# Performance work log

Measured on AMD Instinct MI355X. Metric: run time of the kernel, lower is better.

The kernel has to match this reference:

```python
import jax, jax.numpy as jnp
import numpy as np

B, N, F, H = 2, 2048, 1024, 16
HD = F // H
SQRT_D = float(np.sqrt(F))  # note: module scales by sqrt(in_c), not sqrt(head_dim)


def setup_inputs() -> dict:
    key = jax.random.key(0)
    ks = jax.random.split(key, 9)
    s = 1.0 / np.sqrt(F)
    mk = lambda k: jax.random.uniform(k, (F, F), jnp.float32, -s, s)
    mb = lambda k: jax.random.uniform(k, (F,), jnp.float32, -s, s)
    return {
        "x": jax.random.normal(ks[0], (B, N, F), jnp.float32),
        "Wq": mk(ks[1]), "bq": mb(ks[2]),
        "Wk": mk(ks[3]), "bk": mb(ks[4]),
        "Wv": mk(ks[5]), "bv": mb(ks[6]),
        "Wo": mk(ks[7]), "bo": mb(ks[8]),
    }


def reference(x, Wq, bq, Wk, bk, Wv, bv, Wo, bo):
    b, n, f = x.shape
    # projections (torch Linear: x @ W.T + b); view to (b, n, h, hd)
    q = (x @ Wq.T + bq).reshape(b, n, H, HD)
    k = (x @ Wk.T + bk).reshape(b, n, H, HD)
    v = (x @ Wv.T + bv).reshape(b, n, H, HD)
    score = jnp.einsum('bihd,bjhd->bhij', q, k)
    attn = jax.nn.softmax(score / SQRT_D, axis=-1)
    o = jnp.einsum('bhij,bjhd->bihd', attn, v).reshape(b, n, f)
    return o @ Wo.T + bo
```

## Files before the change

### kernel.cpp

```cpp
#include <hip/hip_runtime.h>
#include <hip/hip_bf16.h>
#include <stdint.h>
#include <stddef.h>

typedef __bf16 bf16;
typedef __attribute__((ext_vector_type(8))) __bf16 bf16x8;
typedef __attribute__((ext_vector_type(4))) __bf16 bf16x4;
typedef __attribute__((ext_vector_type(2))) __bf16 bf16x2;
typedef __attribute__((ext_vector_type(4))) float f32x4;

#define MFMA16(a, b, c) __builtin_amdgcn_mfma_f32_16x16x32_bf16(a, b, c, 0, 0, 0)

#define BB 2
#define SEQ 2048
#define FDIM 1024
#define NH 16
#define HD 64
#define M_TOK 4096
#define N_QKV 3072

#define CSC 0.04508422f

__device__ __forceinline__ void gll16(const bf16* g, bf16* l) {
    __builtin_amdgcn_global_load_lds(
        (const __attribute__((address_space(1))) void*)g,
        (__attribute__((address_space(3))) void*)l, 16, 0, 0);
}

__device__ __forceinline__ bf16 pack_bf16(float f) {
    uint32_t u = __builtin_bit_cast(uint32_t, f);
    uint16_t h = (uint16_t)((u + 0x8000u) >> 16);
    return __builtin_bit_cast(bf16, h);
}

__device__ __forceinline__ uint32_t pk2(float a, float b) {
#if __has_builtin(__builtin_amdgcn_cvt_pk_bf16_f32)
    bf16x2 t = __builtin_amdgcn_cvt_pk_bf16_f32(a, b);
    return __builtin_bit_cast(uint32_t, t);
#else
    uint32_t ua = __builtin_bit_cast(uint32_t, a) + 0x8000u;
    uint32_t ub = __builtin_bit_cast(uint32_t, b) + 0x8000u;
    return __builtin_amdgcn_perm(ub, ua, 0x07060302);
#endif
}

__global__ __launch_bounds__(256) void convert_k(
    const float* __restrict__ x,
    const float* __restrict__ Wq, const float* __restrict__ bq,
    const float* __restrict__ Wk, const float* __restrict__ bk,
    const float* __restrict__ Wv, const float* __restrict__ bv,
    const float* __restrict__ Wo,
    bf16* __restrict__ xb, bf16* __restrict__ Wcat, bf16* __restrict__ Wob,
    float* __restrict__ bcat)
{
    const int tid = blockIdx.x * blockDim.x + threadIdx.x;
    const int nt = gridDim.x * blockDim.x;
    const int NX4 = M_TOK * FDIM / 4;
    const int NW4 = FDIM * FDIM / 4;

    for (int i = tid; i < NX4; i += nt) {
        float4 v = ((const float4*)x)[i];
        bf16x4 o; o[0] = (bf16)v.x; o[1] = (bf16)v.y; o[2] = (bf16)v.z; o[3] = (bf16)v.w;
        ((bf16x4*)xb)[i] = o;
    }
    for (int i = tid; i < NW4; i += nt) {
        float4 v = ((const float4*)Wq)[i];
        bf16x4 o;
        o[0] = (bf16)(v.x * CSC); o[1] = (bf16)(v.y * CSC);
        o[2] = (bf16)(v.z * CSC); o[3] = (bf16)(v.w * CSC);
        ((bf16x4*)Wcat)[i] = o;
        v = ((const float4*)Wk)[i];
        o[0] = (bf16)v.x; o[1] = (bf16)v.y; o[2] = (bf16)v.z; o[3] = (bf16)v.w;
        ((bf16x4*)Wcat)[NW4 + i] = o;
        v = ((const float4*)Wv)[i];
        o[0] = (bf16)v.x; o[1] = (bf16)v.y; o[2] = (bf16)v.z; o[3] = (bf16)v.w;
        ((bf16x4*)Wcat)[2 * NW4 + i] = o;
        v = ((const float4*)Wo)[i];
        o[0] = (bf16)v.x; o[1] = (bf16)v.y; o[2] = (bf16)v.z; o[3] = (bf16)v.w;
        ((bf16x4*)Wob)[i] = o;
    }
    for (int i = tid; i < FDIM; i += nt) {
        bcat[i] = bq[i] * CSC;
        bcat[FDIM + i] = bk[i];
        bcat[2 * FDIM + i] = bv[i];
    }
}

template<int MT>
__global__ __launch_bounds__(256) void gemm_bt(
    const bf16* __restrict__ A,
    const bf16* __restrict__ Bw,
    const float* __restrict__ bias,
    bf16* __restrict__ Cb,
    float* __restrict__ Cf,
    bf16* __restrict__ VtOut,
    int M, int N, int K)
{
    constexpr int RI = MT / 32;
    __shared__ __align__(16) bf16 As[2][MT * 32];
    __shared__ __align__(16) bf16 Bs[2][128 * 32];

    const int tid = threadIdx.x;
    const int lane = tid & 63;
    const int wave = tid >> 6;
    const int m0 = blockIdx.y * MT;
    const int n0 = blockIdx.x * 128;
    const int wm = (wave >> 1) * (MT / 2);
    const int wn = (wave & 1) * 64;
    const int lrow = lane & 15;
    const int lk8 = (lane >> 4) * 8;

    f32x4 acc[RI][4] = {};

    const int srow = wave * 16 + (lane >> 2);
    const int scol = (lane & 3) * 8;
    const bf16* Ag = A + (size_t)(m0 + srow) * K + scol;
    const bf16* Bg = Bw + (size_t)(n0 + srow) * K + scol;
    const int wo = (wave * 16) * 32;

    gll16(Ag, &As[0][wo]);
    if (MT == 128) gll16(Ag + (size_t)64 * K, &As[0][wo + 2048]);
    gll16(Bg, &Bs[0][wo]);
    gll16(Bg + (size_t)64 * K, &Bs[0][wo + 2048]);

    for (int k0 = 0, it = 0; k0 < K; k0 += 32, ++it) {
        const int cur = it & 1;
        __syncthreads();

        if (k0 + 32 < K) {
            const int nxt = cur ^ 1;
            gll16(Ag + k0 + 32, &As[nxt][wo]);
            if (MT == 128) gll16(Ag + (size_t)64 * K + k0 + 32, &As[nxt][wo + 2048]);
            gll16(Bg + k0 + 32, &Bs[nxt][wo]);
            gll16(Bg + (size_t)64 * K + k0 + 32, &Bs[nxt][wo + 2048]);
        }

        bf16x8 af[RI], bfr[4];
#pragma unroll
        for (int s = 0; s < RI; ++s)
            af[s] = *(const bf16x8*)&As[cur][(wm + s * 16 + lrow) * 32 + lk8];
#pragma unroll
        for (int s = 0; s < 4; ++s)
            bfr[s] = *(const bf16x8*)&Bs[cur][(wn + s * 16 + lrow) * 32 + lk8];
#pragma unroll
        for (int i = 0; i < RI; ++i)
#pragma unroll
            for (int j = 0; j < 4; ++j)
                acc[i][j] = MFMA16(af[i], bfr[j], acc[i][j]);
    }

    const int r0 = (lane >> 4) * 4;
    if (MT == 128 && VtOut && n0 >= 2048) {
        const int bql = (m0 >> 11);
#pragma unroll
        for (int i = 0; i < RI; ++i) {
#pragma unroll
            for (int j = 0; j < 4; ++j) {
                const int col = n0 + wn + j * 16 + lrow;
                const float bsv = bias[col];
                const int vh = col - 2048;
                const int row = m0 + wm + i * 16 + r0;
                const int jj = row & (SEQ - 1);
                const int g = jj & 63;
                const int jj2 = (jj & ~63) | ((g >> 5) << 5)
                              | (((g >> 2) & 3) << 3) | (((g >> 4) & 1) << 2);
                bf16x4 vv;
#pragma unroll
                for (int r = 0; r < 4; ++r)
                    vv[r] = pack_bf16(acc[i][j][r] + bsv);
                *(bf16x4*)&VtOut[((size_t)bql * 16 * 64 + vh) * SEQ + jj2] = vv;
            }
        }
        return;
    }
#pragma unroll
    for (int i = 0; i < RI; ++i) {
#pragma unroll
        for (int j = 0; j < 4; ++j) {
            const int col = n0 + wn + j * 16 + lrow;
            const float bsv = bias[col];
#pragma unroll
            for (int r = 0; r < 4; ++r) {
                const int row = m0 + wm + i * 16 + r0 + r;
                const float v = acc[i][j][r] + bsv;
                if (Cb) Cb[(size_t)row * N + col] = pack_bf16(v);
                else    Cf[(size_t)row * N + col] = v;
            }
        }
    }
}

__global__ __launch_bounds__(256) void attn_k(
    const bf16* __restrict__ QKV,
    const bf16* __restrict__ Vt,
    bf16* __restrict__ O)
{
    const int bx = blockIdx.x;
    const int bh = (bx & 7) + 8 * ((bx >> 3) & 3);
    const int qblk = bx >> 5;
    const int b = bh >> 4;
    const int h = bh & 15;
    const int lane = threadIdx.x & 63;
    const int wave = threadIdx.x >> 6;
    const int lrow = lane & 15;
    const int quad = lane >> 4;
    const int lk8 = quad * 8;

    __shared__ __align__(16) bf16 Ks[2][2][128 * 32];
    __shared__ __align__(16) bf16 Vs[2][4][64 * 32];

    const size_t base = (size_t)b * SEQ * N_QKV;
    const bf16* Qp = QKV + base + h * HD;
    const bf16* Kp = QKV + base + FDIM + h * HD;
    const bf16* Vtp = Vt + (size_t)bh * HD * SEQ;

    const int qr0 = qblk * 128 + wave * 32;

    bf16x8 qf[2][2];
#pragma unroll
    for (int qt = 0; qt < 2; ++qt)
#pragma unroll
        for (int ks = 0; ks < 2; ++ks)
            qf[qt][ks] = *(const bf16x8*)(Qp + (size_t)(qr0 + qt * 16 + lrow) * N_QKV
                                          + ks * 32 + lk8);

    bf16x8 ones8;
#pragma unroll
    for (int e = 0; e < 8; ++e) ones8[e] = (bf16)1.0f;

    const f32x4 zf = {0.f, 0.f, 0.f, 0.f};

    f32x4 o[2][4] = {};
    f32x4 o4[2] = {};

    const int srow = wave * 16 + (lane >> 2);
    const int scol = (lane & 3) * 8;
    const bf16* kg = Kp + (size_t)srow * N_QKV + scol;
    const bf16* vg = Vtp + (size_t)srow * SEQ + scol;
    const int wo = (wave * 16) * 32;

    gll16(kg, &Ks[0][0][wo]);
    gll16(kg + 32, &Ks[0][1][wo]);
    gll16(kg + (size_t)64 * N_QKV, &Ks[0][0][wo + 2048]);
    gll16(kg + (size_t)64 * N_QKV + 32, &Ks[0][1][wo + 2048]);
    gll16(vg, &Vs[0][0][wo]);
    gll16(vg + 32, &Vs[0][1][wo]);
    gll16(vg + 64, &Vs[0][2][wo]);
    gll16(vg + 96, &Vs[0][3][wo]);
    kg += (size_t)128 * N_QKV;
    vg += 128;

    for (int jt = 0; jt < SEQ / 128; ++jt) {
        const int cur = jt & 1;
        __syncthreads();

        if (jt + 1 < SEQ / 128) {
            const int nxt = cur ^ 1;
            gll16(kg, &Ks[nxt][0][wo]);
            gll16(kg + 32, &Ks[nxt][1][wo]);
            gll16(kg + (size_t)64 * N_QKV, &Ks[nxt][0][wo + 2048]);
            gll16(kg + (size_t)64 * N_QKV + 32, &Ks[nxt][1][wo + 2048]);
            gll16(vg, &Vs[nxt][0][wo]);
            gll16(vg + 32, &Vs[nxt][1][wo]);
            gll16(vg + 64, &Vs[nxt][2][wo]);
            gll16(vg + 96, &Vs[nxt][3][wo]);
            kg += (size_t)128 * N_QKV;
            vg += 128;
        }

#pragma unroll
        for (int p = 0; p < 4; ++p) {
            f32x4 Sp[2][2];
            __builtin_amdgcn_s_setprio(1);
#pragma unroll
            for (int m = 0; m < 2; ++m) {
                const int jn = 2 * p + m;
                bf16x8 kb0 = *(const bf16x8*)&Ks[cur][0][(jn * 16 + lrow) * 32 + lk8];
                bf16x8 kb1 = *(const bf16x8*)&Ks[cur][1][(jn * 16 + lrow) * 32 + lk8];
                Sp[m][0] = MFMA16(kb0, qf[0][0], zf);
                Sp[m][0] = MFMA16(kb1, qf[0][1], Sp[m][0]);
                Sp[m][1] = MFMA16(kb0, qf[1][0], zf);
                Sp[m][1] = MFMA16(kb1, qf[1][1], Sp[m][1]);
            }
            __builtin_amdgcn_s_setprio(0);

            union { bf16x8 v; uint32_t d[4]; } pb[2];
#pragma unroll
            for (int qt = 0; qt < 2; ++qt) {
                const f32x4 s0 = Sp[0][qt];
                const f32x4 s1 = Sp[1][qt];
                pb[qt].d[0] = pk2(__builtin_amdgcn_exp2f(s0[0]),
                                  __builtin_amdgcn_exp2f(s0[1]));
                pb[qt].d[1] = pk2(__builtin_amdgcn_exp2f(s0[2]),
                                  __builtin_amdgcn_exp2f(s0[3]));
                pb[qt].d[2] = pk2(__builtin_amdgcn_exp2f(s1[0]),
                                  __builtin_amdgcn_exp2f(s1[1]));
                pb[qt].d[3] = pk2(__builtin_amdgcn_exp2f(s1[2]),
                                  __builtin_amdgcn_exp2f(s1[3]));
            }

            __builtin_amdgcn_s_setprio(1);
            o4[0] = MFMA16(ones8, pb[0].v, o4[0]);
            o4[1] = MFMA16(ones8, pb[1].v, o4[1]);
#pragma unroll
            for (int df = 0; df < 4; ++df) {
                bf16x8 vA = *(const bf16x8*)&Vs[cur][p][(df * 16 + lrow) * 32 + lk8];
                o[0][df] = MFMA16(vA, pb[0].v, o[0][df]);
                o[1][df] = MFMA16(vA, pb[1].v, o[1][df]);
            }
            __builtin_amdgcn_s_setprio(0);
        }
    }

#pragma unroll
    for (int qt = 0; qt < 2; ++qt) {
        const float inv = 1.0f / o4[qt][0];
        const int q = qr0 + qt * 16 + lrow;
#pragma unroll
        for (int df = 0; df < 4; ++df) {
            bf16x4 vv;
#pragma unroll
            for (int r = 0; r < 4; ++r)
                vv[r] = pack_bf16(o[qt][df][r] * inv);
            *(bf16x4*)&O[(size_t)(b * SEQ + q) * FDIM + h * HD + df * 16 + quad * 4] = vv;
        }
    }
}

extern "C" void kernel_launch(void* const* d_in, const int* in_sizes, int n_in,
                              void* d_out, int out_size, void* d_ws, size_t ws_size,
                              hipStream_t stream) {
    (void)in_sizes; (void)n_in; (void)out_size; (void)ws_size;
    const float* x  = (const float*)d_in[0];
    const float* Wq = (const float*)d_in[1];
    const float* bq = (const float*)d_in[2];
    const float* Wk = (const float*)d_in[3];
    const float* bk = (const float*)d_in[4];
    const float* Wv = (const float*)d_in[5];
    const float* bv = (const float*)d_in[6];
    const float* Wo = (const float*)d_in[7];
    const float* bo = (const float*)d_in[8];
    float* out = (float*)d_out;

    char* ws = (char*)d_ws;
    bf16* xb    = (bf16*)(ws);
    bf16* Wcat  = (bf16*)(ws + 8388608);
    bf16* Wob   = (bf16*)(ws + 14680064);
    float* bcat = (float*)(ws + 16777216);
    bf16* QKV   = (bf16*)(ws + 16789504);
    bf16* Vt    = (bf16*)(ws + 41955328);
    bf16* Ob    = xb;

    convert_k<<<dim3(1024), dim3(256), 0, stream>>>(x, Wq, bq, Wk, bk, Wv, bv, Wo,
                                                    xb, Wcat, Wob, bcat);
    gemm_bt<128><<<dim3(N_QKV / 128, M_TOK / 128), dim3(256), 0, stream>>>(
        xb, Wcat, bcat, QKV, nullptr, Vt, M_TOK, N_QKV, FDIM);
    attn_k<<<dim3((SEQ / 128) * BB * NH), dim3(256), 0, stream>>>(QKV, Vt, Ob);
    gemm_bt<64><<<dim3(FDIM / 128, M_TOK / 64), dim3(256), 0, stream>>>(
        Ob, Wob, bo, nullptr, out, nullptr, M_TOK, FDIM, FDIM);
}
```

Before: 190.5 us.

## Split attention key range across two wave groups with LDS reduction

The attention block grows from 4 to 8 waves. Each query group of 32 rows is now handled by two waves that each process half of the 32-key sub-tiles in every 128-key tile. The partial outputs and denominators are then combined through shared memory at the end. Cooperative K/V loads are redistributed so each wave issues half as many global-to-LDS loads. The goal is more waves per CU for latency hiding, at the cost of a final LDS reduction and synchronisation, plus register pressure from the launch bounds.

```diff
diff --git a/kernel.cpp b/kernel.cpp
--- a/kernel.cpp
+++ b/kernel.cpp
@@ -190,7 +190,7 @@
     }
 }
 
-__global__ __launch_bounds__(256) void attn_k(
+__global__ __launch_bounds__(512, 4) void attn_k(
     const bf16* __restrict__ QKV,
     const bf16* __restrict__ Vt,
     bf16* __restrict__ O)
@@ -202,6 +202,8 @@
     const int h = bh & 15;
     const int lane = threadIdx.x & 63;
     const int wave = threadIdx.x >> 6;
+    const int qg = wave & 3;
+    const int jp = wave >> 2;
     const int lrow = lane & 15;
     const int quad = lane >> 4;
     const int lk8 = quad * 8;
@@ -214,7 +216,7 @@
     const bf16* Kp = QKV + base + FDIM + h * HD;
     const bf16* Vtp = Vt + (size_t)bh * HD * SEQ;
 
-    const int qr0 = qblk * 128 + wave * 32;
+    const int qr0 = qblk * 128 + qg * 32;
 
     bf16x8 qf[2][2];
 #pragma unroll
@@ -236,17 +238,14 @@
     const int srow = wave * 16 + (lane >> 2);
     const int scol = (lane & 3) * 8;
     const bf16* kg = Kp + (size_t)srow * N_QKV + scol;
-    const bf16* vg = Vtp + (size_t)srow * SEQ + scol;
-    const int wo = (wave * 16) * 32;
-
-    gll16(kg, &Ks[0][0][wo]);
-    gll16(kg + 32, &Ks[0][1][wo]);
-    gll16(kg + (size_t)64 * N_QKV, &Ks[0][0][wo + 2048]);
-    gll16(kg + (size_t)64 * N_QKV + 32, &Ks[0][1][wo + 2048]);
-    gll16(vg, &Vs[0][0][wo]);
-    gll16(vg + 32, &Vs[0][1][wo]);
-    gll16(vg + 64, &Vs[0][2][wo]);
-    gll16(vg + 96, &Vs[0][3][wo]);
+    const int vsrow = qg * 16 + (lane >> 2);
+    const bf16* vg = Vtp + (size_t)vsrow * SEQ + jp * 32 + scol;
+    const int kwo = wave * 512;
+
+    gll16(kg,      &Ks[0][0][0] + kwo);
+    gll16(kg + 32, &Ks[0][1][0] + kwo);
+    gll16(vg,      &Vs[0][0][0] + kwo);
+    gll16(vg + 64, &Vs[0][2][0] + kwo);
     kg += (size_t)128 * N_QKV;
     vg += 128;
 
@@ -256,20 +255,17 @@
 
         if (jt + 1 < SEQ / 128) {
             const int nxt = cur ^ 1;
-            gll16(kg, &Ks[nxt][0][wo]);
-            gll16(kg + 32, &Ks[nxt][1][wo]);
-            gll16(kg + (size_t)64 * N_QKV, &Ks[nxt][0][wo + 2048]);
-            gll16(kg + (size_t)64 * N_QKV + 32, &Ks[nxt][1][wo + 2048]);
-            gll16(vg, &Vs[nxt][0][wo]);
-            gll16(vg + 32, &Vs[nxt][1][wo]);
-            gll16(vg + 64, &Vs[nxt][2][wo]);
-            gll16(vg + 96, &Vs[nxt][3][wo]);
+            gll16(kg,      &Ks[nxt][0][0] + kwo);
+            gll16(kg + 32, &Ks[nxt][1][0] + kwo);
+            gll16(vg,      &Vs[nxt][0][0] + kwo);
+            gll16(vg + 64, &Vs[nxt][2][0] + kwo);
             kg += (size_t)128 * N_QKV;
             vg += 128;
         }
 
 #pragma unroll
-        for (int p = 0; p < 4; ++p) {
+        for (int pp = 0; pp < 2; ++pp) {
+            const int p = (pp << 1) | jp;
             f32x4 Sp[2][2];
             __builtin_amdgcn_s_setprio(1);
 #pragma unroll
@@ -312,9 +308,35 @@
         }
     }
 
+    __syncthreads();
+    float* shO = (float*)Ks;
+    float* shS = (float*)Vs;
+    if (jp == 1) {
+#pragma unroll
+        for (int qt = 0; qt < 2; ++qt)
+#pragma unroll
+            for (int df = 0; df < 4; ++df)
+                *(f32x4*)&shO[((((qt * 4 + df) * 4) + qg) * 64 + lane) * 4] = o[qt][df];
+        shS[(qg * 64 + lane) * 2 + 0] = o4[0][0];
+        shS[(qg * 64 + lane) * 2 + 1] = o4[1][0];
+    }
+    __syncthreads();
+    if (jp == 1) return;
+
+#pragma unroll
+    for (int qt = 0; qt < 2; ++qt)
+#pragma unroll
+        for (int df = 0; df < 4; ++df) {
+            f32x4 t = *(const f32x4*)&shO[((((qt * 4 + df) * 4) + qg) * 64 + lane) * 4];
+            o[qt][df][0] += t[0]; o[qt][df][1] += t[1];
+            o[qt][df][2] += t[2]; o[qt][df][3] += t[3];
+        }
+    const float den0 = o4[0][0] + shS[(qg * 64 + lane) * 2 + 0];
+    const float den1 = o4[1][0] + shS[(qg * 64 + lane) * 2 + 1];
+
 #pragma unroll
     for (int qt = 0; qt < 2; ++qt) {
-        const float inv = 1.0f / o4[qt][0];
+        const float inv = 1.0f / (qt ? den1 : den0);
         const int q = qr0 + qt * 16 + lrow;
 #pragma unroll
         for (int df = 0; df < 4; ++df) {
@@ -355,7 +377,7 @@
                                                     xb, Wcat, Wob, bcat);
     gemm_bt<128><<<dim3(N_QKV / 128, M_TOK / 128), dim3(256), 0, stream>>>(
         xb, Wcat, bcat, QKV, nullptr, Vt, M_TOK, N_QKV, FDIM);
-    attn_k<<<dim3((SEQ / 128) * BB * NH), dim3(256), 0, stream>>>(QKV, Vt, Ob);
+    attn_k<<<dim3((SEQ / 128) * BB * NH), dim3(512), 0, stream>>>(QKV, Vt, Ob);
     gemm_bt<64><<<dim3(FDIM / 128, M_TOK / 64), dim3(256), 0, stream>>>(
         Ob, Wob, bo, nullptr, out, nullptr, M_TOK, FDIM, FDIM);
 }
```

Result: faster. 186.1 us (-2.3%).
